# Performance work log

Measured on AMD Instinct MI355X. Metric: run time of the kernel, lower is better.

## Reference

```python
import jax, jax.numpy as jnp
import numpy as np

B, T, D, H = 4, 2048, 1024, 16
HD = D // H  # head dim = 64


def setup_inputs() -> dict:
    key = jax.random.key(0)
    ks = jax.random.split(key, 6)
    s = 0.02
    return {
        "x": jax.random.normal(ks[0], (B, T, D), dtype=jnp.float32),
        "Wk": jax.random.normal(ks[1], (D, D), dtype=jnp.float32) * s,
        "Wq": jax.random.normal(ks[2], (D, D), dtype=jnp.float32) * s,
        "Wv": jax.random.normal(ks[3], (D, D), dtype=jnp.float32) * s,
        "Wp": jax.random.normal(ks[4], (D, D), dtype=jnp.float32) * s,
        "bp": jnp.zeros((D,), dtype=jnp.float32),
    }


def reference(x, Wk, Wq, Wv, Wp, bp):
    # nn.Linear applies x @ W.T; weights here are stored torch-style [out, in]
    Bq, Tq, _ = x.shape
    k = (x @ Wk.T).reshape(Bq, Tq, H, HD).transpose(0, 2, 1, 3)  # [B,H,T,hd]
    q = (x @ Wq.T).reshape(Bq, Tq, H, HD).transpose(0, 2, 1, 3)
    v = (x @ Wv.T).reshape(Bq, Tq, H, HD).transpose(0, 2, 1, 3)
    scale = HD ** -0.5
    attn = jnp.einsum('bhqd,bhkd->bhqk', q, k) * scale  # [B,H,T,T]
    causal = jnp.tril(jnp.ones((Tq, Tq), dtype=bool))
    attn = jnp.where(causal, attn, -jnp.inf)
    attn = jax.nn.softmax(attn, axis=-1)
    # dropout p=0.0 -> identity (eval semantics)
    out = jnp.einsum('bhqk,bhkd->bhqd', attn, v)  # [B,H,T,hd]
    out = out.transpose(0, 2, 1, 3).reshape(Bq, Tq, D)
    return out @ Wp.T + bp
```

## Files before the change

kernel.cpp:

```cpp
#include <hip/hip_runtime.h>
#include <hip/hip_bf16.h>
#include <stdint.h>


typedef __bf16 bf16x8 __attribute__((ext_vector_type(8)));
typedef float floatx4 __attribute__((ext_vector_type(4)));
typedef unsigned short ushort_t;
typedef unsigned short ushortx8 __attribute__((ext_vector_type(8)));
typedef unsigned short ushortx4 __attribute__((ext_vector_type(4)));
typedef short shortx4 __attribute__((ext_vector_type(4)));

#define MFMA16(a, b, c) __builtin_amdgcn_mfma_f32_16x16x32_bf16((a), (b), (c), 0, 0, 0)
#define MFMA16K16(a, b, c) __builtin_amdgcn_mfma_f32_16x16x16bf16_1k((a), (b), (c), 0, 0, 0)
#define EXP2F(x) __builtin_amdgcn_exp2f(x)

static __device__ __forceinline__ ushort_t f2bfu(float f) {
  union { float f; unsigned u; } v; v.f = f;
  unsigned r = v.u + 0x7FFFu + ((v.u >> 16) & 1u);
  return (ushort_t)(r >> 16);
}

static __device__ __forceinline__ unsigned pack_bf2(float lo, float hi) {
  return __builtin_amdgcn_perm(__float_as_uint(hi), __float_as_uint(lo), 0x07060302);
}

static __device__ __forceinline__ void gl_lds16(const void* g, void* l) {
  __builtin_amdgcn_global_load_lds(
      (const __attribute__((address_space(1))) void*)g,
      (__attribute__((address_space(3))) void*)l, 16, 0, 0);
}

__global__ void cvt_all(const float* __restrict__ x,  const float* __restrict__ wk,
                        const float* __restrict__ wq, const float* __restrict__ wv,
                        const float* __restrict__ wp, ushortx4* __restrict__ dst) {
  const int i = blockIdx.x * blockDim.x + threadIdx.x;
  const float4* src; int off;
  if (i < 2097152) { src = (const float4*)x; off = i; }
  else {
    const int r = i - 2097152;
    const int sel = r >> 18;
    off = r & 262143;
    src = (const float4*)(sel == 0 ? wk : sel == 1 ? wq : sel == 2 ? wv : wp);
  }
  const float4 f = src[off];
  ushortx4 o;
  o[0] = f2bfu(f.x); o[1] = f2bfu(f.y); o[2] = f2bfu(f.z); o[3] = f2bfu(f.w);
  dst[i] = o;
}

__global__ __launch_bounds__(256) void gemm_qkv(
    const ushort_t* __restrict__ X,
    const ushort_t* __restrict__ Wq, const ushort_t* __restrict__ Wk,
    const ushort_t* __restrict__ Wv,
    ushort_t* __restrict__ qb, ushort_t* __restrict__ kb, ushort_t* __restrict__ vtb)
{
  const int z = blockIdx.z;
  const ushort_t* Bm = (z == 0) ? Wq : (z == 1) ? Wk : Wv;
  __shared__ ushort_t Al[128 * 64];
  __shared__ ushort_t Bl[128 * 64];
  const int tid = threadIdx.x;
  const int w = tid >> 6, lane = tid & 63, g = lane >> 4, c = lane & 15;
  const int wm = w >> 1, wn = w & 1;
  const int cswz = c & 7;
  const int m0 = blockIdx.x * 128, n0 = blockIdx.y * 128;

  floatx4 acc[4][4];
  const floatx4 zero4 = {0.f, 0.f, 0.f, 0.f};
#pragma unroll
  for (int i = 0; i < 4; ++i)
#pragma unroll
    for (int j = 0; j < 4; ++j) acc[i][j] = zero4;

  const int srow = tid >> 3;
  const int gsw  = ((tid & 7) ^ (srow & 7)) * 8;

  for (int k0 = 0; k0 < 1024; k0 += 64) {
#pragma unroll
    for (int p = 0; p < 4; ++p) {
      const int row = p * 32 + srow;
      gl_lds16(&X [(size_t)(m0 + row) * 1024 + k0 + gsw], &Al[p * 2048 + tid * 8]);
      gl_lds16(&Bm[(size_t)(n0 + row) * 1024 + k0 + gsw], &Bl[p * 2048 + tid * 8]);
    }
    __syncthreads();
#pragma unroll
    for (int kk = 0; kk < 2; ++kk) {
      bf16x8 af[4], bfr[4];
#pragma unroll
      for (int i = 0; i < 4; ++i) {
        const int sw = ((kk * 4 + g) ^ cswz) * 8;
        af[i]  = *reinterpret_cast<const bf16x8*>(&Al[(wm * 64 + i * 16 + c) * 64 + sw]);
        bfr[i] = *reinterpret_cast<const bf16x8*>(&Bl[(wn * 64 + i * 16 + c) * 64 + sw]);
      }
#pragma unroll
      for (int i = 0; i < 4; ++i)
#pragma unroll
        for (int j = 0; j < 4; ++j)
          acc[i][j] = MFMA16(af[i], bfr[j], acc[i][j]);
    }
    __syncthreads();
  }

#pragma unroll
  for (int i = 0; i < 4; ++i) {
#pragma unroll
    for (int j = 0; j < 4; ++j) {
      const int mbase = m0 + wm * 64 + i * 16 + g * 4;
      const int n = n0 + wn * 64 + j * 16 + c;
      const int h = n >> 6, d = n & 63;
      if (z == 2) {
        const int bb = mbase >> 11, t = mbase & 2047;
        ushortx4 pk;
#pragma unroll
        for (int r = 0; r < 4; ++r) pk[r] = f2bfu(acc[i][j][r]);
        *reinterpret_cast<ushortx4*>(&vtb[(size_t)((bb * 16 + h) * 64 + d) * 2048 + t]) = pk;
      } else {
        ushort_t* ob = (z == 0) ? qb : kb;
#pragma unroll
        for (int r = 0; r < 4; ++r) {
          const int m = mbase + r;
          const int bb = m >> 11, t = m & 2047;
          ob[(size_t)((bb * 16 + h) * 2048 + t) * 64 + d] = f2bfu(acc[i][j][r]);
        }
      }
    }
  }
}

__global__ __launch_bounds__(256, 4) void attn_kernel(
    const ushort_t* __restrict__ qbuf, const ushort_t* __restrict__ kbuf,
    const ushort_t* __restrict__ vtbuf, ushort_t* __restrict__ obuf)
{
  const int j = blockIdx.x, h = blockIdx.y, b = blockIdx.z;
  const int tid = threadIdx.x, w = tid >> 6, lane = tid & 63, g = lane >> 4, c = lane & 15;

  __shared__ ushort_t Kl[128 * 64];
  __shared__ ushort_t Vl[64 * 128];

  const size_t bh = (size_t)(b * 16 + h);
  const ushort_t* kb_bh = kbuf + bh * 2048 * 64;
  const ushort_t* vt_bh = vtbuf + bh * 64 * 2048;
  const ushort_t* qb_bh = qbuf + bh * 2048 * 64;

  const int rb0 = j * 64 + w * 16;
  const int rb1 = (31 - j) * 64 + w * 16;

  bf16x8 aq0[2], aq1[2];
  {
    const ushort_t* qp0 = qb_bh + (size_t)(rb0 + c) * 64;
    aq0[0] = *reinterpret_cast<const bf16x8*>(qp0 + g * 8);
    aq0[1] = *reinterpret_cast<const bf16x8*>(qp0 + 32 + g * 8);
    const ushort_t* qp1 = qb_bh + (size_t)(rb1 + c) * 64;
    aq1[0] = *reinterpret_cast<const bf16x8*>(qp1 + g * 8);
    aq1[1] = *reinterpret_cast<const bf16x8*>(qp1 + 32 + g * 8);
  }

  floatx4 oacc0[4], oacc1[4];
  float l0 = 0.f, l1 = 0.f;
  const floatx4 zero4 = {0.f, 0.f, 0.f, 0.f};
#pragma unroll
  for (int td = 0; td < 4; ++td) { oacc0[td] = zero4; oacc1[td] = zero4; }

  const int krow_s = tid >> 3;
  const int kgsw   = ((tid & 7) ^ (krow_s & 7)) * 8;
  const int vrow_s = tid >> 4;
  const int vgsw   = ((tid & 15) ^ (vrow_s & 15)) * 8;

  const float SCALE = 0.18033688011112042f;

  const int n128 = (33 - j) >> 1;
  for (int kt = 0; kt < n128; ++kt) {
    const int key0 = kt * 128;
#pragma unroll
    for (int p = 0; p < 4; ++p) {
      const int kr = p * 32 + krow_s;
      gl_lds16(&kb_bh[(size_t)(key0 + kr) * 64 + kgsw], &Kl[p * 2048 + tid * 8]);
      const int vr = p * 16 + vrow_s;
      gl_lds16(&vt_bh[(size_t)vr * 2048 + key0 + vgsw], &Vl[p * 2048 + tid * 8]);
    }
    __syncthreads();

#pragma unroll
    for (int s = 0; s < 2; ++s) {
      const int ti = 2 * kt + s;
      const int key0s = ti * 64;
#pragma unroll
      for (int grp = 0; grp < 2; ++grp) {
        const int lim = (grp == 0) ? j : 31 - j;
        if (ti > lim) continue;
        const int rb = (grp == 0) ? rb0 : rb1;
        const bf16x8 b0 = (grp == 0) ? aq0[0] : aq1[0];
        const bf16x8 b1 = (grp == 0) ? aq0[1] : aq1[1];

        float pv[4][4];
#pragma unroll
        for (int t4 = 0; t4 < 4; ++t4) {
          const int krow = s * 64 + t4 * 16 + c;
          const bf16x8 k0f = *reinterpret_cast<const bf16x8*>(&Kl[krow * 64 + ((g) ^ (c & 7)) * 8]);
          const bf16x8 k1f = *reinterpret_cast<const bf16x8*>(&Kl[krow * 64 + ((4 + g) ^ (c & 7)) * 8]);
          floatx4 sa = zero4;
          sa = MFMA16(k0f, b0, sa);
          sa = MFMA16(k1f, b1, sa);
          if (ti == lim) {
            const int q = rb + c;
#pragma unroll
            for (int r = 0; r < 4; ++r) {
              const int key = key0s + t4 * 16 + g * 4 + r;
              const float e = EXP2F(sa[r] * SCALE);
              pv[t4][r] = (key <= q) ? e : 0.f;
            }
          } else {
#pragma unroll
            for (int r = 0; r < 4; ++r) pv[t4][r] = EXP2F(sa[r] * SCALE);
          }
        }
        float lsum = 0.f;
#pragma unroll
        for (int t4 = 0; t4 < 4; ++t4)
          lsum += (pv[t4][0] + pv[t4][1]) + (pv[t4][2] + pv[t4][3]);
        if (grp == 0) l0 += lsum; else l1 += lsum;

#pragma unroll
        for (int t4 = 0; t4 < 4; ++t4) {
          union { unsigned u[2]; shortx4 v; } pk;
          pk.u[0] = pack_bf2(pv[t4][0], pv[t4][1]);
          pk.u[1] = pack_bf2(pv[t4][2], pv[t4][3]);
          const int cc = s * 8 + t4 * 2 + (g >> 1);
          const int ko = (g & 1) * 4;
#pragma unroll
          for (int td = 0; td < 4; ++td) {
            const shortx4 va = *reinterpret_cast<const shortx4*>(
                &Vl[(td * 16 + c) * 128 + (cc ^ c) * 8 + ko]);
            if (grp == 0) oacc0[td] = MFMA16K16(va, pk.v, oacc0[td]);
            else          oacc1[td] = MFMA16K16(va, pk.v, oacc1[td]);
          }
        }
      }
    }
    __syncthreads();
  }

#pragma unroll
  for (int grp = 0; grp < 2; ++grp) {
    float ls = (grp == 0) ? l0 : l1;
    ls += __shfl_xor(ls, 16, 64);
    ls += __shfl_xor(ls, 32, 64);
    const float inv = 1.f / ls;
    const int q = ((grp == 0) ? rb0 : rb1) + c;
    ushort_t* ob = &obuf[((size_t)(b * 2048 + q) * 16 + h) * 64];
#pragma unroll
    for (int td = 0; td < 4; ++td) {
      const floatx4 oa = (grp == 0) ? oacc0[td] : oacc1[td];
      ushortx4 pk;
#pragma unroll
      for (int r = 0; r < 4; ++r) pk[r] = f2bfu(oa[r] * inv);
      *reinterpret_cast<ushortx4*>(&ob[td * 16 + g * 4]) = pk;
    }
  }
}

__global__ __launch_bounds__(256) void gemm_proj(
    const ushort_t* __restrict__ A, const ushort_t* __restrict__ Wp,
    const float* __restrict__ bias, float* __restrict__ out)
{
  __shared__ ushort_t Al[128 * 64];
  __shared__ ushort_t Bl[128 * 64];
  const int tid = threadIdx.x;
  const int w = tid >> 6, lane = tid & 63, g = lane >> 4, c = lane & 15;
  const int wm = w >> 1, wn = w & 1;
  const int cswz = c & 7;
  const int m0 = blockIdx.x * 128, n0 = blockIdx.y * 128;

  floatx4 acc[4][4];
  const floatx4 zero4 = {0.f, 0.f, 0.f, 0.f};
#pragma unroll
  for (int i = 0; i < 4; ++i)
#pragma unroll
    for (int j = 0; j < 4; ++j) acc[i][j] = zero4;

  const int srow = tid >> 3;
  const int gsw  = ((tid & 7) ^ (srow & 7)) * 8;

  for (int k0 = 0; k0 < 1024; k0 += 64) {
#pragma unroll
    for (int p = 0; p < 4; ++p) {
      const int row = p * 32 + srow;
      gl_lds16(&A [(size_t)(m0 + row) * 1024 + k0 + gsw], &Al[p * 2048 + tid * 8]);
      gl_lds16(&Wp[(size_t)(n0 + row) * 1024 + k0 + gsw], &Bl[p * 2048 + tid * 8]);
    }
    __syncthreads();
#pragma unroll
    for (int kk = 0; kk < 2; ++kk) {
      bf16x8 af[4], bfr[4];
#pragma unroll
      for (int i = 0; i < 4; ++i) {
        const int sw = ((kk * 4 + g) ^ cswz) * 8;
        af[i]  = *reinterpret_cast<const bf16x8*>(&Al[(wm * 64 + i * 16 + c) * 64 + sw]);
        bfr[i] = *reinterpret_cast<const bf16x8*>(&Bl[(wn * 64 + i * 16 + c) * 64 + sw]);
      }
#pragma unroll
      for (int i = 0; i < 4; ++i)
#pragma unroll
        for (int j = 0; j < 4; ++j)
          acc[i][j] = MFMA16(af[i], bfr[j], acc[i][j]);
    }
    __syncthreads();
  }

#pragma unroll
  for (int i = 0; i < 4; ++i) {
#pragma unroll
    for (int j = 0; j < 4; ++j) {
      const int n = n0 + wn * 64 + j * 16 + c;
      const float bv = bias[n];
#pragma unroll
      for (int r = 0; r < 4; ++r) {
        const int m = m0 + wm * 64 + i * 16 + g * 4 + r;
        out[(size_t)m * 1024 + n] = acc[i][j][r] + bv;
      }
    }
  }
}

extern "C" void kernel_launch(void* const* d_in, const int* in_sizes, int n_in,
                              void* d_out, int out_size, void* d_ws, size_t ws_size,
                              hipStream_t stream) {
  const float* x  = (const float*)d_in[0];
  const float* Wk = (const float*)d_in[1];
  const float* Wq = (const float*)d_in[2];
  const float* Wv = (const float*)d_in[3];
  const float* Wp = (const float*)d_in[4];
  const float* bp = (const float*)d_in[5];
  float* out = (float*)d_out;

  char* ws = (char*)d_ws;
  const size_t SZ_X = (size_t)8192 * 1024 * 2;
  const size_t SZ_W = (size_t)1024 * 1024 * 2;
  ushort_t* xb    = (ushort_t*)ws;  ws += SZ_X;
  ushort_t* wkb   = (ushort_t*)ws;  ws += SZ_W;
  ushort_t* wqb   = (ushort_t*)ws;  ws += SZ_W;
  ushort_t* wvb   = (ushort_t*)ws;  ws += SZ_W;
  ushort_t* wpb   = (ushort_t*)ws;  ws += SZ_W;
  ushort_t* qbuf  = (ushort_t*)ws;  ws += SZ_X;
  ushort_t* kbuf  = (ushort_t*)ws;  ws += SZ_X;
  ushort_t* vtbuf = (ushort_t*)ws;  ws += SZ_X;
  ushort_t* obuf  = xb;

  cvt_all<<<12288, 256, 0, stream>>>(x, Wk, Wq, Wv, Wp, (ushortx4*)xb);

  gemm_qkv<<<dim3(64, 8, 3), 256, 0, stream>>>(xb, wqb, wkb, wvb, qbuf, kbuf, vtbuf);
  attn_kernel<<<dim3(16, 16, 4), 256, 0, stream>>>(qbuf, kbuf, vtbuf, obuf);
  gemm_proj<<<dim3(64, 8), 256, 0, stream>>>(obuf, wpb, bp, out);
}
```

Baseline: 251.4 us.

## Remap block indices for XCD-aware L2 locality and hoist V fragment loads

Remaps linear block IDs in all three kernels so that consecutive blocks, which the hardware round-robins across the 8 XCDs, land on tiles that share operands within one XCD's L2. This targets redundant HBM traffic for weights and K/V. In attention, the V fragments are loaded once per 64-key subtile and shared by both query groups instead of being reloaded per group. Subtiles past both limits are skipped early, and the occupancy hint rises from 4 to 5 waves. The hoisted vf array adds register pressure, which may conflict with the higher occupancy target.

```diff
diff --git a/kernel.cpp b/kernel.cpp
--- a/kernel.cpp
+++ b/kernel.cpp
@@ -54,7 +54,13 @@
     const ushort_t* __restrict__ Wv,
     ushort_t* __restrict__ qb, ushort_t* __restrict__ kb, ushort_t* __restrict__ vtb)
 {
-  const int z = blockIdx.z;
+  const int L = (int)(blockIdx.x + 64 * (blockIdx.y + 8 * blockIdx.z));
+  const int rr = L & 7, mm = L >> 3;
+  const int m0 = (rr + 8 * (mm & 7)) * 128;
+  const int rest = mm >> 3;
+  const int n0 = (rest & 7) * 128;
+  const int z = rest >> 3;
+
   const ushort_t* Bm = (z == 0) ? Wq : (z == 1) ? Wk : Wv;
   __shared__ ushort_t Al[128 * 64];
   __shared__ ushort_t Bl[128 * 64];
@@ -62,7 +68,6 @@
   const int w = tid >> 6, lane = tid & 63, g = lane >> 4, c = lane & 15;
   const int wm = w >> 1, wn = w & 1;
   const int cswz = c & 7;
-  const int m0 = blockIdx.x * 128, n0 = blockIdx.y * 128;
 
   floatx4 acc[4][4];
   const floatx4 zero4 = {0.f, 0.f, 0.f, 0.f};
@@ -126,11 +131,16 @@
   }
 }
 
-__global__ __launch_bounds__(256, 4) void attn_kernel(
+__global__ __launch_bounds__(256, 5) void attn_kernel(
     const ushort_t* __restrict__ qbuf, const ushort_t* __restrict__ kbuf,
     const ushort_t* __restrict__ vtbuf, ushort_t* __restrict__ obuf)
 {
-  const int j = blockIdx.x, h = blockIdx.y, b = blockIdx.z;
+  const int L = (int)(blockIdx.x + 16 * (blockIdx.y + 16 * blockIdx.z));
+  const int rr = L & 7, mm = L >> 3;
+  const int j = mm >> 3;
+  const int bhl = rr * 8 + (mm & 7);
+  const int h = bhl & 15, b = bhl >> 4;
+
   const int tid = threadIdx.x, w = tid >> 6, lane = tid & 63, g = lane >> 4, c = lane & 15;
 
   __shared__ ushort_t Kl[128 * 64];
@@ -182,7 +192,20 @@
 #pragma unroll
     for (int s = 0; s < 2; ++s) {
       const int ti = 2 * kt + s;
+      if (ti > 31 - j) continue;
       const int key0s = ti * 64;
+
+      shortx4 vf[4][4];
+#pragma unroll
+      for (int t4 = 0; t4 < 4; ++t4) {
+        const int cc = s * 8 + t4 * 2 + (g >> 1);
+        const int ko = (g & 1) * 4;
+#pragma unroll
+        for (int td = 0; td < 4; ++td)
+          vf[t4][td] = *reinterpret_cast<const shortx4*>(
+              &Vl[(td * 16 + c) * 128 + ((cc ^ c) & 15) * 8 + ko]);
+      }
+
 #pragma unroll
       for (int grp = 0; grp < 2; ++grp) {
         const int lim = (grp == 0) ? j : 31 - j;
@@ -224,14 +247,10 @@
           union { unsigned u[2]; shortx4 v; } pk;
           pk.u[0] = pack_bf2(pv[t4][0], pv[t4][1]);
           pk.u[1] = pack_bf2(pv[t4][2], pv[t4][3]);
-          const int cc = s * 8 + t4 * 2 + (g >> 1);
-          const int ko = (g & 1) * 4;
 #pragma unroll
           for (int td = 0; td < 4; ++td) {
-            const shortx4 va = *reinterpret_cast<const shortx4*>(
-                &Vl[(td * 16 + c) * 128 + (cc ^ c) * 8 + ko]);
-            if (grp == 0) oacc0[td] = MFMA16K16(va, pk.v, oacc0[td]);
-            else          oacc1[td] = MFMA16K16(va, pk.v, oacc1[td]);
+            if (grp == 0) oacc0[td] = MFMA16K16(vf[t4][td], pk.v, oacc0[td]);
+            else          oacc1[td] = MFMA16K16(vf[t4][td], pk.v, oacc1[td]);
           }
         }
       }
@@ -262,13 +281,17 @@
     const ushort_t* __restrict__ A, const ushort_t* __restrict__ Wp,
     const float* __restrict__ bias, float* __restrict__ out)
 {
+  const int L = (int)(blockIdx.x + 64 * blockIdx.y);
+  const int rr = L & 7, mm = L >> 3;
+  const int m0 = (rr + 8 * (mm & 7)) * 128;
+  const int n0 = (mm >> 3) * 128;
+
   __shared__ ushort_t Al[128 * 64];
   __shared__ ushort_t Bl[128 * 64];
   const int tid = threadIdx.x;
   const int w = tid >> 6, lane = tid & 63, g = lane >> 4, c = lane & 15;
   const int wm = w >> 1, wn = w & 1;
   const int cswz = c & 7;
-  const int m0 = blockIdx.x * 128, n0 = blockIdx.y * 128;
 
   floatx4 acc[4][4];
   const floatx4 zero4 = {0.f, 0.f, 0.f, 0.f};
```

After: 411.1 us. +63.5%, slower.
